# Performance work log

Measured on AMD Instinct MI355X. Metric: run time of the kernel, lower is better.

The kernel has to match this reference:

```python
import jax, jax.numpy as jnp
import numpy as np

N_NODES = 100000
N_EDGES = 1600000
IN_DIM, HID_DIM, OUT_DIM = 128, 128, 64


def setup_inputs() -> dict:
    key = jax.random.key(0)
    k1, k2, k3, k4 = jax.random.split(key, 4)
    x = jax.random.normal(k1, (N_NODES, IN_DIM), dtype=jnp.float32)
    edge_index = jax.random.randint(k2, (2, N_EDGES), 0, N_NODES, dtype=jnp.int32)
    # Glorot-ish init for weights
    W1 = jax.random.normal(k3, (IN_DIM, HID_DIM), dtype=jnp.float32) / np.sqrt(IN_DIM)
    W2 = jax.random.normal(k4, (HID_DIM, OUT_DIM), dtype=jnp.float32) / np.sqrt(HID_DIM)
    b1 = jnp.zeros((HID_DIM,), dtype=jnp.float32)
    b2 = jnp.zeros((OUT_DIM,), dtype=jnp.float32)
    return {"x": x, "edge_index": edge_index, "W1": W1, "b1": b1, "W2": W2, "b2": b2}


def _gcn_norm(edge_index, num_nodes):
    # PyG gcn_norm: add self-loops, symmetric normalization deg^-1/2 A deg^-1/2
    loops = jnp.arange(num_nodes, dtype=edge_index.dtype)
    src = jnp.concatenate([edge_index[0], loops])  # [E+N]
    tgt = jnp.concatenate([edge_index[1], loops])
    deg = jax.ops.segment_sum(jnp.ones_like(tgt, dtype=jnp.float32), tgt,
                              num_segments=num_nodes)
    dinv = jnp.where(deg > 0, jax.lax.rsqrt(deg), 0.0)
    norm = dinv[src] * dinv[tgt]  # [E+N]
    return src, tgt, norm


def _gcn_conv(x, W, b, src, tgt, norm, num_nodes):
    h = x @ W                              # [N, D_out] transform first (GCNConv order)
    msg = norm[:, None] * h[src]           # gather + scale per edge
    agg = jax.ops.segment_sum(msg, tgt, num_segments=num_nodes)  # scatter-add
    return agg + b


def reference(x, edge_index, W1, b1, W2, b2):
    n = x.shape[0]
    src, tgt, norm = _gcn_norm(edge_index, n)
    h = jax.nn.relu(_gcn_conv(x, W1, b1, src, tgt, norm, n))
    out = _gcn_conv(h, W2, b2, src, tgt, norm, n)
    return out
```

## Files before the change

### kernel.cpp

```cpp
#include <hip/hip_runtime.h>


typedef unsigned int uint;
typedef unsigned short ushort;
typedef __attribute__((ext_vector_type(8))) short bf16x8;
typedef __attribute__((ext_vector_type(8))) ushort u16x8;
typedef __attribute__((ext_vector_type(4))) float f32x4;

#define BSHIFT 8
#define MAXBK  512
#define NB     256
#define CAP    8192

__device__ inline ushort f2bf(float f) {
    uint u = __float_as_uint(f);
    return (ushort)((u + 0x7fffu + ((u >> 16) & 1u)) >> 16);
}
__device__ inline float bf_lo(uint u) { return __uint_as_float(u << 16); }
__device__ inline float bf_hi(uint u) { return __uint_as_float(u & 0xffff0000u); }

__global__ __launch_bounds__(256) void hist_kernel(const int* __restrict__ tgt,
                                                   int* __restrict__ counts,
                                                   int E, int chunk, int nbk) {
    __shared__ int hist[MAXBK];
    int t = threadIdx.x, b = blockIdx.x;
    for (int i = t; i < nbk; i += 256) hist[i] = 0;
    __syncthreads();
    int s = b * chunk, e = min(E, s + chunk);
    int i = s + t * 4;
    for (; i + 3 < e; i += 1024) {
        int4 tv = *(const int4*)&tgt[i];
        atomicAdd(&hist[tv.x >> BSHIFT], 1);
        atomicAdd(&hist[tv.y >> BSHIFT], 1);
        atomicAdd(&hist[tv.z >> BSHIFT], 1);
        atomicAdd(&hist[tv.w >> BSHIFT], 1);
    }
    if (i < e)
        for (int k = i; k < e; ++k) atomicAdd(&hist[tgt[k] >> BSHIFT], 1);
    __syncthreads();
    for (int i2 = t; i2 < nbk; i2 += 256) counts[i2 * NB + b] = hist[i2];
}

__global__ __launch_bounds__(256) void scan_partial(const int* __restrict__ in,
                                                    int* __restrict__ bsum, int M) {
    int t = threadIdx.x, b = blockIdx.x;
    int base = b * 1024 + t * 4;
    int s = 0;
#pragma unroll
    for (int k = 0; k < 4; ++k) s += (base + k < M) ? in[base + k] : 0;
#pragma unroll
    for (int off = 32; off > 0; off >>= 1) s += __shfl_down(s, off, 64);
    __shared__ int ws[4];
    if ((t & 63) == 0) ws[t >> 6] = s;
    __syncthreads();
    if (t == 0) bsum[b] = ws[0] + ws[1] + ws[2] + ws[3];
}

__global__ __launch_bounds__(256) void scan_final_counts(int* __restrict__ counts,
                                                         const int* __restrict__ bsum,
                                                         int M) {
    int t = threadIdx.x, b = blockIdx.x;
    int lane = t & 63, wid = t >> 6;
    int p = 0;
    for (int i = t; i < b; i += 256) p += bsum[i];
#pragma unroll
    for (int off = 32; off > 0; off >>= 1) p += __shfl_down(p, off, 64);
    __shared__ int ps[4];
    if (lane == 0) ps[wid] = p;
    __syncthreads();
    int pre = ps[0] + ps[1] + ps[2] + ps[3];

    int base = b * 1024 + t * 4;
    int d[4];
#pragma unroll
    for (int k = 0; k < 4; ++k) d[k] = (base + k < M) ? counts[base + k] : 0;
    int tot = d[0] + d[1] + d[2] + d[3];
    int incl = tot;
#pragma unroll
    for (int off = 1; off < 64; off <<= 1) {
        int u = __shfl_up(incl, off, 64);
        if (lane >= off) incl += u;
    }
    __shared__ int wsum[4];
    if (lane == 63) wsum[wid] = incl;
    __syncthreads();
    int woff = 0;
    for (int w = 0; w < wid; ++w) woff += wsum[w];
    int run = incl - tot + woff + pre;
#pragma unroll
    for (int k = 0; k < 4; ++k) {
        if (base + k < M) counts[base + k] = run;
        run += d[k];
    }
}

__global__ __launch_bounds__(256) void bucket_scatter(const int* __restrict__ src,
                                                      const int* __restrict__ tgt,
                                                      const int* __restrict__ offsets,
                                                      int* __restrict__ tmpP,
                                                      int E, int chunk, int nbk) {
    __shared__ int cur[MAXBK];
    int t = threadIdx.x, b = blockIdx.x;
    for (int i = t; i < nbk; i += 256) cur[i] = offsets[i * NB + b];
    __syncthreads();
    int s = b * chunk, e = min(E, s + chunk);
    int i = s + t * 4;
    for (; i + 3 < e; i += 1024) {
        int4 sv = *(const int4*)&src[i];
        int4 tv = *(const int4*)&tgt[i];
        int p0 = atomicAdd(&cur[tv.x >> BSHIFT], 1);
        tmpP[p0] = (sv.x << BSHIFT) | (tv.x & 255);
        int p1 = atomicAdd(&cur[tv.y >> BSHIFT], 1);
        tmpP[p1] = (sv.y << BSHIFT) | (tv.y & 255);
        int p2 = atomicAdd(&cur[tv.z >> BSHIFT], 1);
        tmpP[p2] = (sv.z << BSHIFT) | (tv.z & 255);
        int p3 = atomicAdd(&cur[tv.w >> BSHIFT], 1);
        tmpP[p3] = (sv.w << BSHIFT) | (tv.w & 255);
    }
    if (i < e) {
        for (int k = i; k < e; ++k) {
            int tg = tgt[k];
            int p = atomicAdd(&cur[tg >> BSHIFT], 1);
            tmpP[p] = (src[k] << BSHIFT) | (tg & 255);
        }
    }
}

__global__ __launch_bounds__(256) void bucket_finish(const int* __restrict__ tmpP,
                                                     const int* __restrict__ offsets,
                                                     int* __restrict__ rowptr,
                                                     float* __restrict__ dinv,
                                                     int* __restrict__ csr_src,
                                                     int N, int E, int nbk) {
    __shared__ int stage[CAP];
    __shared__ int cnt[256];
    __shared__ int wsum[4];
    int t = threadIdx.x, b = blockIdx.x;
    cnt[t] = 0;
    __syncthreads();
    int s = offsets[b * NB];
    int e = (b + 1 < nbk) ? offsets[(b + 1) * NB] : E;
    int m = e - s;
    for (int i = t; i < m; i += 256) {
        int ed = tmpP[s + i];
        if (i < CAP) stage[i] = ed;
        atomicAdd(&cnt[ed & 255], 1);
    }
    __syncthreads();
    int lane = t & 63, wid = t >> 6;
    int d = cnt[t];
    int incl = d;
#pragma unroll
    for (int off = 1; off < 64; off <<= 1) {
        int u = __shfl_up(incl, off, 64);
        if (lane >= off) incl += u;
    }
    if (lane == 63) wsum[wid] = incl;
    __syncthreads();
    int woff = 0;
    for (int w = 0; w < wid; ++w) woff += wsum[w];
    int excl = s + incl - d + woff;
    int node = b * 256 + t;
    if (node < N) {
        rowptr[node] = excl;
        dinv[node] = rsqrtf((float)d + 1.0f);
    }
    if (b == nbk - 1 && t == 255) rowptr[N] = E;
    cnt[t] = excl;
    __syncthreads();
    for (int i = t; i < m; i += 256) {
        int ed = (i < CAP) ? stage[i] : tmpP[s + i];
        int p = atomicAdd(&cnt[ed & 255], 1);
        csr_src[p] = ed >> BSHIFT;
    }
}

template <int M, typename AT>
__global__ __launch_bounds__(256) void gemm_mfma(const AT* __restrict__ A,
                                                 const float* __restrict__ W,
                                                 const float* __restrict__ dinv,
                                                 ushort* __restrict__ C, int N) {
    constexpr int WTS = 136;
    __shared__ ushort WT[M * WTS];
    __shared__ ushort AS[64 * 136];
    const int tid = threadIdx.x;
    const int R0 = blockIdx.x * 64;
    for (int i = tid; i < 128 * (M / 4); i += 256) {
        int k = i / (M / 4);
        int n0 = (i % (M / 4)) * 4;
        float4 w = *(const float4*)&W[k * M + n0];
        WT[(n0 + 0) * WTS + k] = f2bf(w.x);
        WT[(n0 + 1) * WTS + k] = f2bf(w.y);
        WT[(n0 + 2) * WTS + k] = f2bf(w.z);
        WT[(n0 + 3) * WTS + k] = f2bf(w.w);
    }
    if constexpr (sizeof(AT) == 4) {
#pragma unroll
        for (int g = tid; g < 2048; g += 256) {
            int row = g >> 5;
            int col = (g & 31) * 4;
            int ar = min(R0 + row, N - 1);
            float4 v = *(const float4*)&((const float*)A)[(size_t)ar * 128 + col];
            ushort* d = &AS[row * 136 + col];
            d[0] = f2bf(v.x); d[1] = f2bf(v.y);
            d[2] = f2bf(v.z); d[3] = f2bf(v.w);
        }
    } else {
#pragma unroll
        for (int g = tid; g < 1024; g += 256) {
            int row = g >> 4;
            int col = (g & 15) * 8;
            int ar = min(R0 + row, N - 1);
            u16x8 v = *(const u16x8*)&((const ushort*)A)[(size_t)ar * 128 + col];
            *(u16x8*)&AS[row * 136 + col] = v;
        }
    }
    __syncthreads();

    const int wv = tid >> 6, lane = tid & 63;
    const int quad = lane >> 4, mrow = lane & 15;

    f32x4 acc[M / 16];
#pragma unroll
    for (int t = 0; t < M / 16; ++t) acc[t] = (f32x4){0.f, 0.f, 0.f, 0.f};

#pragma unroll
    for (int ks = 0; ks < 4; ++ks) {
        const int k0 = ks * 32 + quad * 8;
        bf16x8 af = *(const bf16x8*)&AS[(wv * 16 + mrow) * 136 + k0];
#pragma unroll
        for (int t = 0; t < M / 16; ++t) {
            bf16x8 bfr = *(const bf16x8*)&WT[(t * 16 + mrow) * WTS + k0];
            acc[t] = __builtin_amdgcn_mfma_f32_16x16x32_bf16(af, bfr, acc[t], 0, 0, 0);
        }
    }

    const int orow0 = R0 + wv * 16 + quad * 4;
#pragma unroll
    for (int r = 0; r < 4; ++r) {
        int orow = orow0 + r;
        if (orow < N) {
            float dv = dinv[orow];
#pragma unroll
            for (int t = 0; t < M / 16; ++t)
                C[(size_t)orow * M + t * 16 + mrow] = f2bf(dv * acc[t][r]);
        }
    }
}

template <int D, bool RELU, bool OUTBF>
__global__ __launch_bounds__(256) void gather_kernel(
    const ushort* __restrict__ h, const int* __restrict__ rowptr,
    const int* __restrict__ csr_src, const float* __restrict__ dinv,
    const float* __restrict__ bias, void* __restrict__ outv, int N) {
    constexpr int Q = D / 8;
    constexpr int G = 64 / Q;
    const int wid = threadIdx.x >> 6, lane = threadIdx.x & 63;
    const int node = blockIdx.x * 4 + wid;
    if (node >= N) return;
    const int g = lane / Q, q = lane % Q;
    const int qoff = q * 8;
    const int beg = rowptr[node], end = rowptr[node + 1];
    float acc[8] = {};

    int j = beg;
    for (; j + 2 * G <= end; j += 2 * G) {
        int s0 = csr_src[j + g];
        int s1 = csr_src[j + G + g];
        uint4 va = *(const uint4*)&h[(size_t)s0 * D + qoff];
        uint4 vb = *(const uint4*)&h[(size_t)s1 * D + qoff];
        acc[0] += bf_lo(va.x); acc[1] += bf_hi(va.x);
        acc[2] += bf_lo(va.y); acc[3] += bf_hi(va.y);
        acc[4] += bf_lo(va.z); acc[5] += bf_hi(va.z);
        acc[6] += bf_lo(va.w); acc[7] += bf_hi(va.w);
        acc[0] += bf_lo(vb.x); acc[1] += bf_hi(vb.x);
        acc[2] += bf_lo(vb.y); acc[3] += bf_hi(vb.y);
        acc[4] += bf_lo(vb.z); acc[5] += bf_hi(vb.z);
        acc[6] += bf_lo(vb.w); acc[7] += bf_hi(vb.w);
    }
    if (j < end) {
        int e0 = j + g, e1 = j + G + g;
        bool v0 = e0 < end, v1 = e1 < end;
        int s0 = v0 ? csr_src[e0] : 0;
        int s1 = v1 ? csr_src[e1] : 0;
        float m0 = v0 ? 1.0f : 0.0f;
        float m1 = v1 ? 1.0f : 0.0f;
        uint4 va = *(const uint4*)&h[(size_t)s0 * D + qoff];
        uint4 vb = *(const uint4*)&h[(size_t)s1 * D + qoff];
        acc[0] += m0 * bf_lo(va.x); acc[1] += m0 * bf_hi(va.x);
        acc[2] += m0 * bf_lo(va.y); acc[3] += m0 * bf_hi(va.y);
        acc[4] += m0 * bf_lo(va.z); acc[5] += m0 * bf_hi(va.z);
        acc[6] += m0 * bf_lo(va.w); acc[7] += m0 * bf_hi(va.w);
        acc[0] += m1 * bf_lo(vb.x); acc[1] += m1 * bf_hi(vb.x);
        acc[2] += m1 * bf_lo(vb.y); acc[3] += m1 * bf_hi(vb.y);
        acc[4] += m1 * bf_lo(vb.z); acc[5] += m1 * bf_hi(vb.z);
        acc[6] += m1 * bf_lo(vb.w); acc[7] += m1 * bf_hi(vb.w);
    }
#pragma unroll
    for (int m2 = Q; m2 < 64; m2 <<= 1)
#pragma unroll
        for (int k = 0; k < 8; ++k) acc[k] += __shfl_xor(acc[k], m2, 64);

    {
        uint4 hv = *(const uint4*)&h[(size_t)node * D + qoff];
        acc[0] += bf_lo(hv.x); acc[1] += bf_hi(hv.x);
        acc[2] += bf_lo(hv.y); acc[3] += bf_hi(hv.y);
        acc[4] += bf_lo(hv.z); acc[5] += bf_hi(hv.z);
        acc[6] += bf_lo(hv.w); acc[7] += bf_hi(hv.w);
    }
    if (g == 0) {
        const float di = dinv[node];
        float4 b0 = *(const float4*)&bias[qoff];
        float4 b1 = *(const float4*)&bias[qoff + 4];
        float r[8] = {di * acc[0] + b0.x, di * acc[1] + b0.y,
                      di * acc[2] + b0.z, di * acc[3] + b0.w,
                      di * acc[4] + b1.x, di * acc[5] + b1.y,
                      di * acc[6] + b1.z, di * acc[7] + b1.w};
        if (RELU) {
#pragma unroll
            for (int k = 0; k < 8; ++k) r[k] = fmaxf(r[k], 0.0f);
        }
        if constexpr (OUTBF) {
            ushort* out = (ushort*)outv;
            u16x8 o;
#pragma unroll
            for (int k = 0; k < 8; ++k) o[k] = f2bf(r[k]);
            *(u16x8*)&out[(size_t)node * D + qoff] = o;
        } else {
            float* out = (float*)outv;
            *(float4*)&out[(size_t)node * D + qoff]     = make_float4(r[0], r[1], r[2], r[3]);
            *(float4*)&out[(size_t)node * D + qoff + 4] = make_float4(r[4], r[5], r[6], r[7]);
        }
    }
}

extern "C" void kernel_launch(void* const* d_in, const int* in_sizes, int n_in,
                              void* d_out, int out_size, void* d_ws, size_t ws_size,
                              hipStream_t stream) {
    const float* x  = (const float*)d_in[0];
    const int*   ei = (const int*)d_in[1];
    const float* W1 = (const float*)d_in[2];
    const float* b1 = (const float*)d_in[3];
    const float* W2 = (const float*)d_in[4];
    const float* b2 = (const float*)d_in[5];
    float* out = (float*)d_out;

    const int N = in_sizes[0] / 128;
    const int E = in_sizes[1] / 2;
    const int* src = ei;
    const int* tgt = ei + E;

    const int nbk   = (N + 255) >> BSHIFT;
    const int chunk = (((E + NB - 1) / NB) + 3) & ~3;
    const int Mc    = nbk * NB;

    float* ws = (float*)d_ws;
    const size_t Np = (size_t)((N + 3) & ~3);
    float*  dinv    = ws;
    int*    rowptr  = (int*)(ws + Np);
    int*    counts  = rowptr + Np + 4;
    int*    bsum    = counts + MAXBK * NB;
    int*    csr_src = bsum + 128;
    int*    tmpP    = csr_src + E;
    ushort* h       = (ushort*)(tmpP + E);
    ushort* h1      = h + (size_t)N * 128;
    ushort* h2      = h;

    const int nbc = (Mc + 1023) / 1024;

    hist_kernel<<<NB, 256, 0, stream>>>(tgt, counts, E, chunk, nbk);
    scan_partial<<<nbc, 256, 0, stream>>>(counts, bsum, Mc);
    scan_final_counts<<<nbc, 256, 0, stream>>>(counts, bsum, Mc);
    bucket_scatter<<<NB, 256, 0, stream>>>(src, tgt, counts, tmpP, E, chunk, nbk);
    bucket_finish<<<nbk, 256, 0, stream>>>(tmpP, counts, rowptr, dinv, csr_src, N, E, nbk);

    gemm_mfma<128, float><<<(N + 63) / 64, 256, 0, stream>>>(x, W1, dinv, h, N);
    gather_kernel<128, true, true><<<(N + 3) / 4, 256, 0, stream>>>(
        h, rowptr, csr_src, dinv, b1, h1, N);

    gemm_mfma<64, ushort><<<(N + 63) / 64, 256, 0, stream>>>(h1, W2, dinv, h2, N);
    gather_kernel<64, false, false><<<(N + 3) / 4, 256, 0, stream>>>(
        h2, rowptr, csr_src, dinv, b2, out, N);
}
```

Baseline: 319.2 us.

## Fuse CSR build into one cooperative kernel and load GEMM A operand directly

Merges histogram, two scan passes, bucket scatter and bucket finish into a single cooperative kernel separated by grid-wide syncs, removing four kernel launches and their gaps. The GEMM no longer stages the A tile through shared memory; each lane loads its A fragment from global memory and converts it to bf16 in registers. The trade-off is grid-sync cost, reduced parallelism in the finish phase (256 blocks looping over buckets), and less coalesced A loads.

```diff
diff --git a/kernel.cpp b/kernel.cpp
--- a/kernel.cpp
+++ b/kernel.cpp
@@ -1,4 +1,7 @@
 #include <hip/hip_runtime.h>
+#include <hip/hip_cooperative_groups.h>
+
+namespace cg = cooperative_groups;
 
 
 typedef unsigned int uint;
@@ -19,159 +22,151 @@
 __device__ inline float bf_lo(uint u) { return __uint_as_float(u << 16); }
 __device__ inline float bf_hi(uint u) { return __uint_as_float(u & 0xffff0000u); }
 
-__global__ __launch_bounds__(256) void hist_kernel(const int* __restrict__ tgt,
-                                                   int* __restrict__ counts,
-                                                   int E, int chunk, int nbk) {
-    __shared__ int hist[MAXBK];
-    int t = threadIdx.x, b = blockIdx.x;
-    for (int i = t; i < nbk; i += 256) hist[i] = 0;
-    __syncthreads();
-    int s = b * chunk, e = min(E, s + chunk);
-    int i = s + t * 4;
-    for (; i + 3 < e; i += 1024) {
-        int4 tv = *(const int4*)&tgt[i];
-        atomicAdd(&hist[tv.x >> BSHIFT], 1);
-        atomicAdd(&hist[tv.y >> BSHIFT], 1);
-        atomicAdd(&hist[tv.z >> BSHIFT], 1);
-        atomicAdd(&hist[tv.w >> BSHIFT], 1);
-    }
-    if (i < e)
-        for (int k = i; k < e; ++k) atomicAdd(&hist[tgt[k] >> BSHIFT], 1);
-    __syncthreads();
-    for (int i2 = t; i2 < nbk; i2 += 256) counts[i2 * NB + b] = hist[i2];
-}
-
-__global__ __launch_bounds__(256) void scan_partial(const int* __restrict__ in,
-                                                    int* __restrict__ bsum, int M) {
-    int t = threadIdx.x, b = blockIdx.x;
-    int base = b * 1024 + t * 4;
-    int s = 0;
-#pragma unroll
-    for (int k = 0; k < 4; ++k) s += (base + k < M) ? in[base + k] : 0;
-#pragma unroll
-    for (int off = 32; off > 0; off >>= 1) s += __shfl_down(s, off, 64);
-    __shared__ int ws[4];
-    if ((t & 63) == 0) ws[t >> 6] = s;
-    __syncthreads();
-    if (t == 0) bsum[b] = ws[0] + ws[1] + ws[2] + ws[3];
-}
-
-__global__ __launch_bounds__(256) void scan_final_counts(int* __restrict__ counts,
-                                                         const int* __restrict__ bsum,
-                                                         int M) {
-    int t = threadIdx.x, b = blockIdx.x;
-    int lane = t & 63, wid = t >> 6;
-    int p = 0;
-    for (int i = t; i < b; i += 256) p += bsum[i];
-#pragma unroll
-    for (int off = 32; off > 0; off >>= 1) p += __shfl_down(p, off, 64);
-    __shared__ int ps[4];
-    if (lane == 0) ps[wid] = p;
-    __syncthreads();
-    int pre = ps[0] + ps[1] + ps[2] + ps[3];
-
-    int base = b * 1024 + t * 4;
-    int d[4];
-#pragma unroll
-    for (int k = 0; k < 4; ++k) d[k] = (base + k < M) ? counts[base + k] : 0;
-    int tot = d[0] + d[1] + d[2] + d[3];
-    int incl = tot;
-#pragma unroll
-    for (int off = 1; off < 64; off <<= 1) {
-        int u = __shfl_up(incl, off, 64);
-        if (lane >= off) incl += u;
-    }
-    __shared__ int wsum[4];
-    if (lane == 63) wsum[wid] = incl;
-    __syncthreads();
-    int woff = 0;
-    for (int w = 0; w < wid; ++w) woff += wsum[w];
-    int run = incl - tot + woff + pre;
-#pragma unroll
-    for (int k = 0; k < 4; ++k) {
-        if (base + k < M) counts[base + k] = run;
-        run += d[k];
-    }
-}
-
-__global__ __launch_bounds__(256) void bucket_scatter(const int* __restrict__ src,
-                                                      const int* __restrict__ tgt,
-                                                      const int* __restrict__ offsets,
-                                                      int* __restrict__ tmpP,
-                                                      int E, int chunk, int nbk) {
-    __shared__ int cur[MAXBK];
-    int t = threadIdx.x, b = blockIdx.x;
-    for (int i = t; i < nbk; i += 256) cur[i] = offsets[i * NB + b];
-    __syncthreads();
-    int s = b * chunk, e = min(E, s + chunk);
-    int i = s + t * 4;
-    for (; i + 3 < e; i += 1024) {
-        int4 sv = *(const int4*)&src[i];
-        int4 tv = *(const int4*)&tgt[i];
-        int p0 = atomicAdd(&cur[tv.x >> BSHIFT], 1);
-        tmpP[p0] = (sv.x << BSHIFT) | (tv.x & 255);
-        int p1 = atomicAdd(&cur[tv.y >> BSHIFT], 1);
-        tmpP[p1] = (sv.y << BSHIFT) | (tv.y & 255);
-        int p2 = atomicAdd(&cur[tv.z >> BSHIFT], 1);
-        tmpP[p2] = (sv.z << BSHIFT) | (tv.z & 255);
-        int p3 = atomicAdd(&cur[tv.w >> BSHIFT], 1);
-        tmpP[p3] = (sv.w << BSHIFT) | (tv.w & 255);
-    }
-    if (i < e) {
-        for (int k = i; k < e; ++k) {
-            int tg = tgt[k];
-            int p = atomicAdd(&cur[tg >> BSHIFT], 1);
-            tmpP[p] = (src[k] << BSHIFT) | (tg & 255);
-        }
-    }
-}
-
-__global__ __launch_bounds__(256) void bucket_finish(const int* __restrict__ tmpP,
-                                                     const int* __restrict__ offsets,
-                                                     int* __restrict__ rowptr,
-                                                     float* __restrict__ dinv,
-                                                     int* __restrict__ csr_src,
-                                                     int N, int E, int nbk) {
+__global__ __launch_bounds__(256) void csr_coop(
+    const int* __restrict__ src, const int* __restrict__ tgt,
+    int* __restrict__ counts, int* __restrict__ bsum,
+    int* __restrict__ rowptr, float* __restrict__ dinv,
+    int* __restrict__ csr_src, int* __restrict__ tmpP,
+    int N, int E, int chunk, int nbk, int Mc, int nbc) {
+    cg::grid_group grid = cg::this_grid();
     __shared__ int stage[CAP];
     __shared__ int cnt[256];
-    __shared__ int wsum[4];
-    int t = threadIdx.x, b = blockIdx.x;
-    cnt[t] = 0;
-    __syncthreads();
-    int s = offsets[b * NB];
-    int e = (b + 1 < nbk) ? offsets[(b + 1) * NB] : E;
-    int m = e - s;
-    for (int i = t; i < m; i += 256) {
-        int ed = tmpP[s + i];
-        if (i < CAP) stage[i] = ed;
-        atomicAdd(&cnt[ed & 255], 1);
-    }
-    __syncthreads();
-    int lane = t & 63, wid = t >> 6;
-    int d = cnt[t];
-    int incl = d;
-#pragma unroll
-    for (int off = 1; off < 64; off <<= 1) {
-        int u = __shfl_up(incl, off, 64);
-        if (lane >= off) incl += u;
-    }
-    if (lane == 63) wsum[wid] = incl;
-    __syncthreads();
-    int woff = 0;
-    for (int w = 0; w < wid; ++w) woff += wsum[w];
-    int excl = s + incl - d + woff;
-    int node = b * 256 + t;
-    if (node < N) {
-        rowptr[node] = excl;
-        dinv[node] = rsqrtf((float)d + 1.0f);
-    }
-    if (b == nbk - 1 && t == 255) rowptr[N] = E;
-    cnt[t] = excl;
-    __syncthreads();
-    for (int i = t; i < m; i += 256) {
-        int ed = (i < CAP) ? stage[i] : tmpP[s + i];
-        int p = atomicAdd(&cnt[ed & 255], 1);
-        csr_src[p] = ed >> BSHIFT;
+    __shared__ int ws4[4];
+    const int t = threadIdx.x, b = blockIdx.x;
+    const int lane = t & 63, wid = t >> 6;
+
+    {
+        int* hist = stage;
+        for (int i = t; i < nbk; i += 256) hist[i] = 0;
+        __syncthreads();
+        int s = b * chunk, e = min(E, s + chunk);
+        int i = s + t * 4;
+        for (; i + 3 < e; i += 1024) {
+            int4 tv = *(const int4*)&tgt[i];
+            atomicAdd(&hist[tv.x >> BSHIFT], 1);
+            atomicAdd(&hist[tv.y >> BSHIFT], 1);
+            atomicAdd(&hist[tv.z >> BSHIFT], 1);
+            atomicAdd(&hist[tv.w >> BSHIFT], 1);
+        }
+        if (i < e)
+            for (int k = i; k < e; ++k) atomicAdd(&hist[tgt[k] >> BSHIFT], 1);
+        __syncthreads();
+        for (int i2 = t; i2 < nbk; i2 += 256) counts[i2 * NB + b] = hist[i2];
+    }
+    grid.sync();
+
+    if (b < nbc) {
+        int base = b * 1024 + t * 4;
+        int s = 0;
+#pragma unroll
+        for (int k = 0; k < 4; ++k) s += (base + k < Mc) ? counts[base + k] : 0;
+#pragma unroll
+        for (int off = 32; off > 0; off >>= 1) s += __shfl_down(s, off, 64);
+        if (lane == 0) ws4[wid] = s;
+        __syncthreads();
+        if (t == 0) bsum[b] = ws4[0] + ws4[1] + ws4[2] + ws4[3];
+    }
+    grid.sync();
+
+    if (b < nbc) {
+        int p = 0;
+        for (int i = t; i < b; i += 256) p += bsum[i];
+#pragma unroll
+        for (int off = 32; off > 0; off >>= 1) p += __shfl_down(p, off, 64);
+        if (lane == 0) cnt[wid] = p;
+        __syncthreads();
+        int pre = cnt[0] + cnt[1] + cnt[2] + cnt[3];
+
+        int base = b * 1024 + t * 4;
+        int d[4];
+#pragma unroll
+        for (int k = 0; k < 4; ++k) d[k] = (base + k < Mc) ? counts[base + k] : 0;
+        int tot = d[0] + d[1] + d[2] + d[3];
+        int incl = tot;
+#pragma unroll
+        for (int off = 1; off < 64; off <<= 1) {
+            int u = __shfl_up(incl, off, 64);
+            if (lane >= off) incl += u;
+        }
+        if (lane == 63) ws4[wid] = incl;
+        __syncthreads();
+        int woff = 0;
+        for (int w = 0; w < wid; ++w) woff += ws4[w];
+        int run = incl - tot + woff + pre;
+#pragma unroll
+        for (int k = 0; k < 4; ++k) {
+            if (base + k < Mc) counts[base + k] = run;
+            run += d[k];
+        }
+    }
+    grid.sync();
+
+    {
+        int* cur = stage;
+        for (int i = t; i < nbk; i += 256) cur[i] = counts[i * NB + b];
+        __syncthreads();
+        int s = b * chunk, e = min(E, s + chunk);
+        int i = s + t * 4;
+        for (; i + 3 < e; i += 1024) {
+            int4 sv = *(const int4*)&src[i];
+            int4 tv = *(const int4*)&tgt[i];
+            int p0 = atomicAdd(&cur[tv.x >> BSHIFT], 1);
+            tmpP[p0] = (sv.x << BSHIFT) | (tv.x & 255);
+            int p1 = atomicAdd(&cur[tv.y >> BSHIFT], 1);
+            tmpP[p1] = (sv.y << BSHIFT) | (tv.y & 255);
+            int p2 = atomicAdd(&cur[tv.z >> BSHIFT], 1);
+            tmpP[p2] = (sv.z << BSHIFT) | (tv.z & 255);
+            int p3 = atomicAdd(&cur[tv.w >> BSHIFT], 1);
+            tmpP[p3] = (sv.w << BSHIFT) | (tv.w & 255);
+        }
+        if (i < e) {
+            for (int k = i; k < e; ++k) {
+                int tg = tgt[k];
+                int p = atomicAdd(&cur[tg >> BSHIFT], 1);
+                tmpP[p] = (src[k] << BSHIFT) | (tg & 255);
+            }
+        }
+    }
+    grid.sync();
+
+    for (int vb = b; vb < nbk; vb += 256) {
+        cnt[t] = 0;
+        __syncthreads();
+        int s = counts[vb * NB];
+        int e = (vb + 1 < nbk) ? counts[(vb + 1) * NB] : E;
+        int m = e - s;
+        for (int i = t; i < m; i += 256) {
+            int ed = tmpP[s + i];
+            if (i < CAP) stage[i] = ed;
+            atomicAdd(&cnt[ed & 255], 1);
+        }
+        __syncthreads();
+        int d = cnt[t];
+        int incl = d;
+#pragma unroll
+        for (int off = 1; off < 64; off <<= 1) {
+            int u = __shfl_up(incl, off, 64);
+            if (lane >= off) incl += u;
+        }
+        if (lane == 63) ws4[wid] = incl;
+        __syncthreads();
+        int woff = 0;
+        for (int w = 0; w < wid; ++w) woff += ws4[w];
+        int excl = s + incl - d + woff;
+        int node = vb * 256 + t;
+        if (node < N) {
+            rowptr[node] = excl;
+            dinv[node] = rsqrtf((float)d + 1.0f);
+        }
+        if (vb == nbk - 1 && t == 255) rowptr[N] = E;
+        cnt[t] = excl;
+        __syncthreads();
+        for (int i = t; i < m; i += 256) {
+            int ed = (i < CAP) ? stage[i] : tmpP[s + i];
+            int p = atomicAdd(&cnt[ed & 255], 1);
+            csr_src[p] = ed >> BSHIFT;
+        }
+        __syncthreads();
     }
 }
 
@@ -182,9 +177,7 @@
                                                  ushort* __restrict__ C, int N) {
     constexpr int WTS = 136;
     __shared__ ushort WT[M * WTS];
-    __shared__ ushort AS[64 * 136];
     const int tid = threadIdx.x;
-    const int R0 = blockIdx.x * 64;
     for (int i = tid; i < 128 * (M / 4); i += 256) {
         int k = i / (M / 4);
         int n0 = (i % (M / 4)) * 4;
@@ -194,31 +187,13 @@
         WT[(n0 + 2) * WTS + k] = f2bf(w.z);
         WT[(n0 + 3) * WTS + k] = f2bf(w.w);
     }
-    if constexpr (sizeof(AT) == 4) {
-#pragma unroll
-        for (int g = tid; g < 2048; g += 256) {
-            int row = g >> 5;
-            int col = (g & 31) * 4;
-            int ar = min(R0 + row, N - 1);
-            float4 v = *(const float4*)&((const float*)A)[(size_t)ar * 128 + col];
-            ushort* d = &AS[row * 136 + col];
-            d[0] = f2bf(v.x); d[1] = f2bf(v.y);
-            d[2] = f2bf(v.z); d[3] = f2bf(v.w);
-        }
-    } else {
-#pragma unroll
-        for (int g = tid; g < 1024; g += 256) {
-            int row = g >> 4;
-            int col = (g & 15) * 8;
-            int ar = min(R0 + row, N - 1);
-            u16x8 v = *(const u16x8*)&((const ushort*)A)[(size_t)ar * 128 + col];
-            *(u16x8*)&AS[row * 136 + col] = v;
-        }
-    }
     __syncthreads();
 
     const int wv = tid >> 6, lane = tid & 63;
     const int quad = lane >> 4, mrow = lane & 15;
+    int arow_i = blockIdx.x * 64 + wv * 16 + mrow;
+    if (arow_i >= N) arow_i = N - 1;
+    const AT* arow = &A[(size_t)arow_i * 128];
 
     f32x4 acc[M / 16];
 #pragma unroll
@@ -227,15 +202,26 @@
 #pragma unroll
     for (int ks = 0; ks < 4; ++ks) {
         const int k0 = ks * 32 + quad * 8;
-        bf16x8 af = *(const bf16x8*)&AS[(wv * 16 + mrow) * 136 + k0];
+        bf16x8 af;
+        if constexpr (sizeof(AT) == 4) {
+            float4 a0 = *(const float4*)&arow[k0];
+            float4 a1 = *(const float4*)&arow[k0 + 4];
+            af[0] = (short)f2bf(a0.x); af[1] = (short)f2bf(a0.y);
+            af[2] = (short)f2bf(a0.z); af[3] = (short)f2bf(a0.w);
+            af[4] = (short)f2bf(a1.x); af[5] = (short)f2bf(a1.y);
+            af[6] = (short)f2bf(a1.z); af[7] = (short)f2bf(a1.w);
+        } else {
+            af = *(const bf16x8*)&arow[k0];
+        }
 #pragma unroll
         for (int t = 0; t < M / 16; ++t) {
-            bf16x8 bfr = *(const bf16x8*)&WT[(t * 16 + mrow) * WTS + k0];
+            int n = t * 16 + mrow;
+            bf16x8 bfr = *(const bf16x8*)&WT[n * WTS + k0];
             acc[t] = __builtin_amdgcn_mfma_f32_16x16x32_bf16(af, bfr, acc[t], 0, 0, 0);
         }
     }
 
-    const int orow0 = R0 + wv * 16 + quad * 4;
+    const int orow0 = blockIdx.x * 64 + wv * 16 + quad * 4;
 #pragma unroll
     for (int r = 0; r < 4; ++r) {
         int orow = orow0 + r;
@@ -353,6 +339,7 @@
     const int nbk   = (N + 255) >> BSHIFT;
     const int chunk = (((E + NB - 1) / NB) + 3) & ~3;
     const int Mc    = nbk * NB;
+    const int nbc   = (Mc + 1023) / 1024;
 
     float* ws = (float*)d_ws;
     const size_t Np = (size_t)((N + 3) & ~3);
@@ -366,13 +353,15 @@
     ushort* h1      = h + (size_t)N * 128;
     ushort* h2      = h;
 
-    const int nbc = (Mc + 1023) / 1024;
-
-    hist_kernel<<<NB, 256, 0, stream>>>(tgt, counts, E, chunk, nbk);
-    scan_partial<<<nbc, 256, 0, stream>>>(counts, bsum, Mc);
-    scan_final_counts<<<nbc, 256, 0, stream>>>(counts, bsum, Mc);
-    bucket_scatter<<<NB, 256, 0, stream>>>(src, tgt, counts, tmpP, E, chunk, nbk);
-    bucket_finish<<<nbk, 256, 0, stream>>>(tmpP, counts, rowptr, dinv, csr_src, N, E, nbk);
+    {
+        int Nc = N, Ec = E, ck = chunk, nb = nbk, mc = Mc, nc = nbc;
+        void* args[] = {(void*)&src, (void*)&tgt, (void*)&counts, (void*)&bsum,
+                        (void*)&rowptr, (void*)&dinv, (void*)&csr_src,
+                        (void*)&tmpP, (void*)&Nc, (void*)&Ec, (void*)&ck,
+                        (void*)&nb, (void*)&mc, (void*)&nc};
+        hipLaunchCooperativeKernel((void*)csr_coop, dim3(NB), dim3(256),
+                                   args, 0, stream);
+    }
 
     gemm_mfma<128, float><<<(N + 63) / 64, 256, 0, stream>>>(x, W1, dinv, h, N);
     gather_kernel<128, true, true><<<(N + 3) / 4, 256, 0, stream>>>(
```

New measurement: 454.4 us. +42.4%, slower.
